# Optimization experiments

Hardware: AMD Instinct MI355X
Metric: run time of the kernel (lower is better)

## Reference

```python
import jax, jax.numpy as jnp
import numpy as np

Z_SIGN = jnp.array([1.0, -1.0], dtype=jnp.float32)  # eigenvalues of Pauli-Z for basis |0>,|1>

def _quanv_features(x, theta):
    """Batched 4-qubit statevector simulation over all 196 patches at once.
    x: [B, 784], theta: [4] RZ angles. Returns [B, 784] features."""
    B = x.shape[0]
    img = x.reshape(B, 28, 28)
    # 2x2 stride-2 patches, row-major within patch: [(r,c),(r,c+1),(r+1,c),(r+1,c+1)]
    patches = img.reshape(B, 14, 2, 14, 2).transpose(0, 1, 3, 2, 4).reshape(B, 196, 4)
    half = 0.5 * patches
    c, s = jnp.cos(half), jnp.sin(half)  # [B,196,4]
    # RY(x_i)|0> = cos(x_i/2)|0> + sin(x_i/2)|1>; product state over 4 wires
    q0 = jnp.stack([c[..., 0], s[..., 0]], -1)
    q1 = jnp.stack([c[..., 1], s[..., 1]], -1)
    q2 = jnp.stack([c[..., 2], s[..., 2]], -1)
    q3 = jnp.stack([c[..., 3], s[..., 3]], -1)
    state = jnp.einsum('bpi,bpj,bpk,bpl->bpijkl', q0, q1, q2, q3).astype(jnp.complex64)
    # RZ(theta_w) = diag(e^{-i t/2}, e^{+i t/2}) on each wire -> single phase tensor [2,2,2,2]
    z = Z_SIGN
    expo = (theta[0] * z[:, None, None, None] + theta[1] * z[None, :, None, None]
            + theta[2] * z[None, None, :, None] + theta[3] * z[None, None, None, :])
    state = state * jnp.exp(-0.5j * expo.astype(jnp.complex64))
    # CNOT(0,1): flip wire-1 axis where wire-0 == 1
    state = jnp.stack([state[:, :, 0], state[:, :, 1, ::-1]], axis=2)
    # CNOT(2,3): flip wire-3 axis where wire-2 == 1
    state = jnp.stack([state[:, :, :, :, 0], state[:, :, :, :, 1, ::-1]], axis=4)
    prob = jnp.abs(state) ** 2  # [B,196,2,2,2,2]
    # <Z_w> per wire
    meas = jnp.stack([
        jnp.sum(prob * z.reshape([1, 1] + [2 if i == w else 1 for i in range(4)]),
                axis=(2, 3, 4, 5))
        for w in range(4)
    ], axis=-1)  # [B,196,4]
    return meas.reshape(B, 196 * 4)

def setup_inputs() -> dict:
    key = jax.random.key(0)
    k1, k2, k3 = jax.random.split(key, 3)
    B = 4096
    x = jax.random.normal(k1, (B, 784), dtype=jnp.float32)
    theta = jax.random.normal(k2, (4,), dtype=jnp.float32) * 0.1  # RZ params of var_layer
    W = jax.random.normal(k3, (10, 784), dtype=jnp.float32) * 0.02  # linear head weight
    b = jnp.zeros((10,), dtype=jnp.float32)
    return {"x": x, "theta": theta, "W": W, "b": b}

def reference(x, theta, W, b):
    feats = _quanv_features(x, theta)          # [B, 784]
    logits = feats @ W.T + b                   # [B, 10]
    return jax.nn.log_softmax(logits, axis=-1)
```

## Files before the change

### kernel.cpp

```cpp
#include <hip/hip_runtime.h>


typedef float f32x4 __attribute__((ext_vector_type(4)));
typedef short s16x8 __attribute__((ext_vector_type(8)));

__device__ __forceinline__ ushort f2bf(float f) {
    unsigned u = __float_as_uint(f);
    u += 0x7fffu + ((u >> 16) & 1u);
    return (ushort)(u >> 16);
}

__global__ __launch_bounds__(512, 2) void quanv_mfma(
    const float* __restrict__ x,
    const float* __restrict__ W,
    const float* __restrict__ bias,
    float* __restrict__ out,
    int B)
{
    __shared__ __align__(16) ushort Wb[16][800];
    __shared__ float Cp[8][16][16];
    __shared__ float bl[16];

    const int tid  = threadIdx.x;
    const int wv   = tid >> 6;
    const int lane = tid & 63;
    const int h    = lane >> 4;
    const int col  = lane & 15;
    const int rbase = blockIdx.x << 4;

    {
        const float4* __restrict__ W4 = reinterpret_cast<const float4*>(W);
        for (int i4 = tid; i4 < 3200; i4 += 512) {
            const int c  = i4 / 200;
            const int k4 = i4 - c * 200;
            ushort4 v = {0, 0, 0, 0};
            if (c < 10 && k4 < 196) {
                const float4 wq = W4[c * 196 + k4];
                v.x = f2bf(wq.x); v.y = f2bf(wq.y);
                v.z = f2bf(wq.z); v.w = f2bf(wq.w);
            }
            *reinterpret_cast<ushort4*>(&Wb[c][k4 << 2]) = v;
        }
        if (tid < 10) bl[tid] = bias[tid];
        if (tid >= 10 && tid < 16) bl[tid] = 0.0f;
    }

    int r = rbase + col;
    if (r >= B) r = B - 1;
    const float* __restrict__ xr = x + (size_t)r * 784;

    __syncthreads();

    f32x4 acc = {0.f, 0.f, 0.f, 0.f};
    for (int t = wv; t < 25; t += 8) {
        const int p0 = 8 * t + 2 * h;
        const bool ok = p0 < 196;
        const int pp = ok ? p0 : 0;
        const int pr = pp / 14;
        const int pc = pp - pr * 14;
        const float4* __restrict__ xp =
            reinterpret_cast<const float4*>(xr + pr * 56 + 2 * pc);
        const float4 top = xp[0];
        const float4 bot = xp[7];
        float f0 = __cosf(top.x), f1 = f0 * __cosf(top.y);
        float f2 = __cosf(bot.x), f3 = f2 * __cosf(bot.y);
        float f4 = __cosf(top.z), f5 = f4 * __cosf(top.w);
        float f6 = __cosf(bot.z), f7 = f6 * __cosf(bot.w);
        if (!ok) { f0=f1=f2=f3=f4=f5=f6=f7=0.f; }
        s16x8 a = { (short)f2bf(f0), (short)f2bf(f1),
                    (short)f2bf(f2), (short)f2bf(f3),
                    (short)f2bf(f4), (short)f2bf(f5),
                    (short)f2bf(f6), (short)f2bf(f7) };
        const s16x8 b = *reinterpret_cast<const s16x8*>(
            &Wb[col][32 * t + (h << 3)]);
        acc = __builtin_amdgcn_mfma_f32_16x16x32_bf16(a, b, acc, 0, 0, 0);
    }

#pragma unroll
    for (int j = 0; j < 4; ++j)
        Cp[wv][(h << 2) + j][col] = acc[j];

    __syncthreads();

    if (tid < 16) {
        const int rr = rbase + tid;
        if (rr < B) {
            float s[10];
#pragma unroll
            for (int c = 0; c < 10; ++c) s[c] = bl[c];
#pragma unroll
            for (int w = 0; w < 8; ++w)
#pragma unroll
                for (int c = 0; c < 10; ++c) s[c] += Cp[w][tid][c];
            float m = s[0];
#pragma unroll
            for (int c = 1; c < 10; ++c) m = fmaxf(m, s[c]);
            float sum = 0.f;
#pragma unroll
            for (int c = 0; c < 10; ++c) sum += __expf(s[c] - m);
            const float lse = m + __logf(sum);
            float* __restrict__ o = out + (size_t)rr * 10;
#pragma unroll
            for (int c = 0; c < 10; ++c) o[c] = s[c] - lse;
        }
    }
}

extern "C" void kernel_launch(void* const* d_in, const int* in_sizes, int n_in,
                              void* d_out, int out_size, void* d_ws, size_t ws_size,
                              hipStream_t stream) {
    const float* x   = (const float*)d_in[0];
    const float* W   = (const float*)d_in[2];
    const float* b   = (const float*)d_in[3];
    float* out       = (float*)d_out;

    const int B = in_sizes[0] / 784;
    const int blocks = (B + 15) / 16;
    quanv_mfma<<<blocks, 512, 0, stream>>>(x, W, b, out, B);
}
```

Measured before the change: 9.724 us.

## Drop LDS weight staging, load W directly, prefetch inputs, parallelize softmax epilogue

```diff
diff --git a/kernel.cpp b/kernel.cpp
--- a/kernel.cpp
+++ b/kernel.cpp
@@ -10,16 +10,14 @@
     return (ushort)(u >> 16);
 }
 
-__global__ __launch_bounds__(512, 2) void quanv_mfma(
+__global__ __launch_bounds__(512) void quanv_mfma(
     const float* __restrict__ x,
     const float* __restrict__ W,
     const float* __restrict__ bias,
     float* __restrict__ out,
     int B)
 {
-    __shared__ __align__(16) ushort Wb[16][800];
     __shared__ float Cp[8][16][16];
-    __shared__ float bl[16];
 
     const int tid  = threadIdx.x;
     const int wv   = tid >> 6;
@@ -28,52 +26,55 @@
     const int col  = lane & 15;
     const int rbase = blockIdx.x << 4;
 
-    {
-        const float4* __restrict__ W4 = reinterpret_cast<const float4*>(W);
-        for (int i4 = tid; i4 < 3200; i4 += 512) {
-            const int c  = i4 / 200;
-            const int k4 = i4 - c * 200;
-            ushort4 v = {0, 0, 0, 0};
-            if (c < 10 && k4 < 196) {
-                const float4 wq = W4[c * 196 + k4];
-                v.x = f2bf(wq.x); v.y = f2bf(wq.y);
-                v.z = f2bf(wq.z); v.w = f2bf(wq.w);
-            }
-            *reinterpret_cast<ushort4*>(&Wb[c][k4 << 2]) = v;
-        }
-        if (tid < 10) bl[tid] = bias[tid];
-        if (tid >= 10 && tid < 16) bl[tid] = 0.0f;
-    }
-
     int r = rbase + col;
     if (r >= B) r = B - 1;
     const float* __restrict__ xr = x + (size_t)r * 784;
+    const int colw = col < 10 ? col : 9;
+    const float* __restrict__ wr = W + colw * 784;
 
-    __syncthreads();
+    float4 xt[4], xb[4], wa[4], wb[4];
+#pragma unroll
+    for (int i = 0; i < 4; ++i) {
+        const int t = wv + 8 * i;
+        if (t < 25) {
+            const int p0 = 8 * t + 2 * h;
+            const bool ok = p0 < 196;
+            const int pp = ok ? p0 : 0;
+            const int pr = pp / 14;
+            const int pc = pp - 14 * pr;
+            const float4* __restrict__ xp =
+                reinterpret_cast<const float4*>(xr + pr * 56 + 2 * pc);
+            xt[i] = xp[0];
+            xb[i] = xp[7];
+            const int k0 = ok ? (32 * t + 8 * h) : 0;
+            const float4* __restrict__ wp =
+                reinterpret_cast<const float4*>(wr + k0);
+            wa[i] = wp[0];
+            wb[i] = wp[1];
+        }
+    }
 
     f32x4 acc = {0.f, 0.f, 0.f, 0.f};
-    for (int t = wv; t < 25; t += 8) {
-        const int p0 = 8 * t + 2 * h;
-        const bool ok = p0 < 196;
-        const int pp = ok ? p0 : 0;
-        const int pr = pp / 14;
-        const int pc = pp - pr * 14;
-        const float4* __restrict__ xp =
-            reinterpret_cast<const float4*>(xr + pr * 56 + 2 * pc);
-        const float4 top = xp[0];
-        const float4 bot = xp[7];
-        float f0 = __cosf(top.x), f1 = f0 * __cosf(top.y);
-        float f2 = __cosf(bot.x), f3 = f2 * __cosf(bot.y);
-        float f4 = __cosf(top.z), f5 = f4 * __cosf(top.w);
-        float f6 = __cosf(bot.z), f7 = f6 * __cosf(bot.w);
-        if (!ok) { f0=f1=f2=f3=f4=f5=f6=f7=0.f; }
-        s16x8 a = { (short)f2bf(f0), (short)f2bf(f1),
-                    (short)f2bf(f2), (short)f2bf(f3),
-                    (short)f2bf(f4), (short)f2bf(f5),
-                    (short)f2bf(f6), (short)f2bf(f7) };
-        const s16x8 b = *reinterpret_cast<const s16x8*>(
-            &Wb[col][32 * t + (h << 3)]);
-        acc = __builtin_amdgcn_mfma_f32_16x16x32_bf16(a, b, acc, 0, 0, 0);
+#pragma unroll
+    for (int i = 0; i < 4; ++i) {
+        const int t = wv + 8 * i;
+        if (t < 25) {
+            const bool ok = (8 * t + 2 * h) < 196;
+            float f0 = __cosf(xt[i].x), f1 = f0 * __cosf(xt[i].y);
+            float f2 = __cosf(xb[i].x), f3 = f2 * __cosf(xb[i].y);
+            float f4 = __cosf(xt[i].z), f5 = f4 * __cosf(xt[i].w);
+            float f6 = __cosf(xb[i].z), f7 = f6 * __cosf(xb[i].w);
+            if (!ok) { f0=f1=f2=f3=f4=f5=f6=f7=0.f; }
+            const s16x8 a = { (short)f2bf(f0), (short)f2bf(f1),
+                              (short)f2bf(f2), (short)f2bf(f3),
+                              (short)f2bf(f4), (short)f2bf(f5),
+                              (short)f2bf(f6), (short)f2bf(f7) };
+            const s16x8 b = { (short)f2bf(wa[i].x), (short)f2bf(wa[i].y),
+                              (short)f2bf(wa[i].z), (short)f2bf(wa[i].w),
+                              (short)f2bf(wb[i].x), (short)f2bf(wb[i].y),
+                              (short)f2bf(wb[i].z), (short)f2bf(wb[i].w) };
+            acc = __builtin_amdgcn_mfma_f32_16x16x32_bf16(a, b, acc, 0, 0, 0);
+        }
     }
 
 #pragma unroll
@@ -82,27 +83,26 @@
 
     __syncthreads();
 
-    if (tid < 16) {
-        const int rr = rbase + tid;
-        if (rr < B) {
-            float s[10];
+    if (tid < 256) {
+        const int row = tid >> 4;
+        const int c   = tid & 15;
+        float s = 0.f;
 #pragma unroll
-            for (int c = 0; c < 10; ++c) s[c] = bl[c];
+        for (int w = 0; w < 8; ++w) s += Cp[w][row][c];
+        const bool cv = c < 10;
+        const float v = cv ? (s + bias[c]) : -3.0e38f;
+        float m = v;
 #pragma unroll
-            for (int w = 0; w < 8; ++w)
+        for (int off = 1; off < 16; off <<= 1)
+            m = fmaxf(m, __shfl_xor(m, off, 64));
+        float e = cv ? __expf(v - m) : 0.f;
 #pragma unroll
-                for (int c = 0; c < 10; ++c) s[c] += Cp[w][tid][c];
-            float m = s[0];
-#pragma unroll
-            for (int c = 1; c < 10; ++c) m = fmaxf(m, s[c]);
-            float sum = 0.f;
-#pragma unroll
-            for (int c = 0; c < 10; ++c) sum += __expf(s[c] - m);
-            const float lse = m + __logf(sum);
-            float* __restrict__ o = out + (size_t)rr * 10;
-#pragma unroll
-            for (int c = 0; c < 10; ++c) o[c] = s[c] - lse;
-        }
+        for (int off = 1; off < 16; off <<= 1)
+            e += __shfl_xor(e, off, 64);
+        const float lse = m + __logf(e);
+        const int rr = rbase + row;
+        if (cv && rr < B)
+            out[(size_t)rr * 10 + c] = v - lse;
     }
 }
 
```

After: 9.729 us. Within noise of the previous version (+0.1%).
